# Kernel optimization log

Hardware: AMD Instinct MI355X
Metric: run time of the kernel (lower is better)

Reference implementation:

```python
import jax, jax.numpy as jnp
import numpy as np
from jax import lax

DN = ('NCH', 'OIH', 'NCH')

def conv1d(x, w, b, pad=0):
    y = lax.conv_general_dilated(x, w, window_strides=(1,), padding=[(pad, pad)], dimension_numbers=DN)
    return y + b[None, :, None]

def conv_transpose1d(x, w_torch, b):
    # torch ConvTranspose1d weight: [C_in, C_out, K]; equivalent to full conv with flipped kernel
    k = w_torch.shape[-1]
    w = jnp.flip(jnp.transpose(w_torch, (1, 0, 2)), axis=-1)  # [C_out, C_in, K]
    y = lax.conv_general_dilated(x, w, window_strides=(1,), padding=[(k - 1, k - 1)], dimension_numbers=DN)
    return y + b[None, :, None]

def converter(signal, w1, b1, w2, b2, wt, bt, w3, b3):
    h = jax.nn.relu(conv1d(signal, w1, b1))          # [B,10,n-2]
    h = jax.nn.relu(conv1d(h, w2, b2))               # [B,10,n-2]
    h = jax.nn.relu(conv_transpose1d(h, wt, bt))     # [B,10,n]
    h = jax.nn.sigmoid(conv1d(h, w3, b3))            # [B,2,n]
    return h

def setup_inputs() -> dict:
    key = jax.random.key(0)
    ks = jax.random.split(key, 12)
    B, C, n = 32, 128, 8192
    signal = jax.random.normal(ks[0], (B, C, n), dtype=jnp.float32)
    curr_diag = jax.random.uniform(ks[1], (B, n - 1), dtype=jnp.float32) + 0.5
    s = 0.1
    return {
        'signal': signal,
        'curr_diag': curr_diag,
        'index_diag': 1,
        'w1': jax.random.normal(ks[2], (10, C, 3), dtype=jnp.float32) * s,
        'b1': jax.random.normal(ks[3], (10,), dtype=jnp.float32) * s,
        'w2': jax.random.normal(ks[4], (10, 10, 1), dtype=jnp.float32) * s,
        'b2': jax.random.normal(ks[5], (10,), dtype=jnp.float32) * s,
        'wt': jax.random.normal(ks[6], (10, 10, 3), dtype=jnp.float32) * s,
        'bt': jax.random.normal(ks[7], (10,), dtype=jnp.float32) * s,
        'w3': jax.random.normal(ks[8], (2, 10, 1), dtype=jnp.float32) * s,
        'b3': jax.random.normal(ks[9], (2,), dtype=jnp.float32) * s,
        'const': jnp.float32(0.99),
    }

def reference(signal, curr_diag, index_diag, w1, b1, w2, b2, wt, bt, w3, b3, const):
    n = signal.shape[-1]
    lr = converter(signal, w1, b1, w2, b2, wt, bt, w3, b3)  # [B,2,n]
    left, right = lr[:, 0, :], lr[:, 1, :]
    # diag_len = n - index_diag; next diag has length diag_len - 1
    mass_in = curr_diag[:, 1:] * right[:, 1:n - index_diag]
    mass_in = mass_in + curr_diag[:, :-1] * left[:, index_diag:n - 1]
    mass_out = right[:, 0:n - index_diag - 1] + left[:, index_diag + 1:n]
    next_diag = const * mass_in / mass_out
    next_diag = jnp.log(next_diag)
    next_diag = next_diag - jnp.mean(next_diag)
    return next_diag
```

## Files before the change

### kernel.cpp

```cpp
#include <hip/hip_runtime.h>
#include <math.h>

#define B    32
#define CIN  128
#define NN   8192
#define N1   8190
#define N1P  8192
#define CH   10

__global__ void k0_prep(const float* __restrict__ w1, float* __restrict__ wT)
{
    const int i = blockIdx.x * 256 + threadIdx.x;
    if (i < CIN * 32) {
        const int ci = i >> 5, r = i & 31;
        float v = 0.f;
        if (r < 30) {
            const int o = r / 3, k = r - o * 3;
            v = w1[(o * CIN + ci) * 3 + k];
        }
        wT[i] = v;
    }
}

__global__ __launch_bounds__(256) void k1_conv12(
    const float* __restrict__ sig, const float* __restrict__ wT, const float* __restrict__ b1,
    const float* __restrict__ w2, const float* __restrict__ b2, float* __restrict__ h2out)
{
    const int tid = threadIdx.x;
    const int b   = blockIdx.y;
    const int t   = blockIdx.x * 256 + tid;
    const int tc  = (t < N1 - 1) ? t : (N1 - 1);
    const float* sp = sig + (size_t)b * CIN * NN + tc;

    float y[CH];
#pragma unroll
    for (int o = 0; o < CH; ++o) y[o] = b1[o];

    float ax[8], ay[8], az[8];
    float bx[8], by[8], bz[8];

    auto load = [&](float* x0, float* x1, float* x2, int c) {
#pragma unroll
        for (int j = 0; j < 8; ++j) {
            const float* p = sp + (size_t)(c * 8 + j) * NN;
            x0[j] = p[0]; x1[j] = p[1]; x2[j] = p[2];
        }
    };
    auto comp = [&](const float* x0, const float* x1, const float* x2, int c) {
        const float* wbase = wT + c * 8 * 32;
#pragma unroll
        for (int j = 0; j < 8; ++j) {
            const float* wrow = wbase + j * 32;
#pragma unroll
            for (int o = 0; o < CH; ++o) {
                y[o] = fmaf(wrow[o * 3 + 0], x0[j], y[o]);
                y[o] = fmaf(wrow[o * 3 + 1], x1[j], y[o]);
                y[o] = fmaf(wrow[o * 3 + 2], x2[j], y[o]);
            }
        }
    };

    load(ax, ay, az, 0);
    for (int c = 0; c < 16; c += 2) {
        load(bx, by, bz, c + 1);
        comp(ax, ay, az, c);
        if (c + 2 < 16) load(ax, ay, az, c + 2);
        comp(bx, by, bz, c + 1);
    }

    if (t < N1) {
#pragma unroll
        for (int o = 0; o < CH; ++o) y[o] = fmaxf(y[o], 0.f);
#pragma unroll
        for (int o = 0; o < CH; ++o) {
            float a = b2[o];
#pragma unroll
            for (int i = 0; i < CH; ++i) a = fmaf(w2[o * CH + i], y[i], a);
            h2out[((size_t)b * CH + o) * N1P + t] = fmaxf(a, 0.f);
        }
    }
}

__global__ __launch_bounds__(256) void k2_fused(
    const float* __restrict__ h2, const float* __restrict__ cd,
    const float* __restrict__ wt, const float* __restrict__ bt,
    const float* __restrict__ w3, const float* __restrict__ b3,
    const float* __restrict__ cstp, float* __restrict__ outv, float* __restrict__ bsums)
{
    __shared__ float lsh[260], rsh[260];
    __shared__ float red[256];
    const int tid = threadIdx.x;
    const int b   = blockIdx.y;
    const int t0  = blockIdx.x * 256;
    const float* hb = h2 + (size_t)b * CH * N1P;

    auto computeLR = [&](int sidx) {
        const int s = t0 + sidx;
        float acc[CH];
#pragma unroll
        for (int o = 0; o < CH; ++o) acc[o] = bt[o];
#pragma unroll
        for (int i = 0; i < CH; ++i) {
            const float* hp = hb + (size_t)i * N1P;
            const float v0 = (s < N1)            ? hp[s]     : 0.f;
            const float v1 = (s >= 1 && s <= N1) ? hp[s - 1] : 0.f;
            const float v2 = (s >= 2)            ? hp[s - 2] : 0.f;
            const float* wp = wt + i * CH * 3;
#pragma unroll
            for (int o = 0; o < CH; ++o) {
                acc[o] = fmaf(wp[o * 3 + 0], v0, acc[o]);
                acc[o] = fmaf(wp[o * 3 + 1], v1, acc[o]);
                acc[o] = fmaf(wp[o * 3 + 2], v2, acc[o]);
            }
        }
        float l = b3[0], r = b3[1];
#pragma unroll
        for (int o = 0; o < CH; ++o) {
            const float h3 = fmaxf(acc[o], 0.f);
            l = fmaf(w3[o],      h3, l);
            r = fmaf(w3[CH + o], h3, r);
        }
        lsh[sidx] = 1.f / (1.f + __expf(-l));
        rsh[sidx] = 1.f / (1.f + __expf(-r));
    };

    computeLR(tid);
    if (tid < 3 && t0 + 256 + tid < NN) computeLR(256 + tid);
    __syncthreads();

    const int t = t0 + tid;
    float v = 0.f;
    if (t < N1) {
        const float c0 = cd[(size_t)b * (NN - 1) + t];
        const float c1 = cd[(size_t)b * (NN - 1) + t + 1];
        const float mi = c1 * rsh[tid + 1] + c0 * lsh[tid + 1];
        const float mo = rsh[tid] + lsh[tid + 2];
        v = __logf(cstp[0] * mi / mo);
        outv[(size_t)b * N1 + t] = v;
    }

    red[tid] = v;
    __syncthreads();
#pragma unroll
    for (int s = 128; s > 0; s >>= 1) {
        if (tid < s) red[tid] += red[tid + s];
        __syncthreads();
    }
    if (tid == 0) bsums[blockIdx.y * gridDim.x + blockIdx.x] = red[0];
}

__global__ __launch_bounds__(256) void k3_meansub(
    const float* __restrict__ bsums, float* __restrict__ outv, int n)
{
    __shared__ float red[256];
    const int tid = threadIdx.x;
    float s = 0.f;
#pragma unroll
    for (int i = 0; i < 4; ++i) s += bsums[tid + i * 256];
    red[tid] = s;
    __syncthreads();
#pragma unroll
    for (int st = 128; st > 0; st >>= 1) {
        if (tid < st) red[tid] += red[tid + st];
        __syncthreads();
    }
    const float mean = red[0] / (float)(B * N1);
    __syncthreads();
    const int i = blockIdx.x * 256 + tid;
    if (i < n) outv[i] -= mean;
}

extern "C" void kernel_launch(void* const* d_in, const int* in_sizes, int n_in,
                              void* d_out, int out_size, void* d_ws, size_t ws_size,
                              hipStream_t stream)
{
    const float* sig = (const float*)d_in[0];
    const float* cd  = (const float*)d_in[1];
    const float* w1  = (const float*)d_in[3];
    const float* b1  = (const float*)d_in[4];
    const float* w2  = (const float*)d_in[5];
    const float* b2  = (const float*)d_in[6];
    const float* wt  = (const float*)d_in[7];
    const float* bt  = (const float*)d_in[8];
    const float* w3  = (const float*)d_in[9];
    const float* b3  = (const float*)d_in[10];
    const float* cst = (const float*)d_in[11];

    float* outv = (float*)d_out;

    float* ws   = (float*)d_ws;
    float* wT   = ws;
    float* h2   = wT + CIN * 32;
    float* bsum = h2 + (size_t)B * CH * N1P;

    dim3 blk(256);
    dim3 g1(32, B);

    k0_prep   <<<dim3(16), blk, 0, stream>>>(w1, wT);
    k1_conv12 <<<g1, blk, 0, stream>>>(sig, wT, b1, w2, b2, h2);
    k2_fused  <<<g1, blk, 0, stream>>>(h2, cd, wt, bt, w3, b3, cst, outv, bsum);
    k3_meansub<<<dim3((out_size + 255) / 256), blk, 0, stream>>>(bsum, outv, out_size);
}
```

Measured before the change: 265.1 us.

## Fuse conv1/conv2 with transpose-conv and output stage using halo tiles in LDS

```diff
diff --git a/kernel.cpp b/kernel.cpp
--- a/kernel.cpp
+++ b/kernel.cpp
@@ -1,12 +1,13 @@
 #include <hip/hip_runtime.h>
 #include <math.h>
 
-#define B    32
-#define CIN  128
-#define NN   8192
-#define N1   8190
-#define N1P  8192
-#define CH   10
+#define B     32
+#define CIN   128
+#define NN    8192
+#define N1    8190
+#define CH    10
+#define TOUT  252
+#define NTILE 33
 
 __global__ void k0_prep(const float* __restrict__ w1, float* __restrict__ wT)
 {
@@ -22,95 +23,81 @@
     }
 }
 
-__global__ __launch_bounds__(256) void k1_conv12(
-    const float* __restrict__ sig, const float* __restrict__ wT, const float* __restrict__ b1,
-    const float* __restrict__ w2, const float* __restrict__ b2, float* __restrict__ h2out)
+__global__ __launch_bounds__(256, 4) void k_main(
+    const float* __restrict__ sig, const float* __restrict__ wT,
+    const float* __restrict__ b1, const float* __restrict__ w2, const float* __restrict__ b2,
+    const float* __restrict__ wt, const float* __restrict__ bt,
+    const float* __restrict__ w3, const float* __restrict__ b3,
+    const float* __restrict__ cd, const float* __restrict__ cstp,
+    float* __restrict__ outv, float* __restrict__ bsums)
 {
+    __shared__ float h2s[CH * 256];
+    __shared__ float lsh[256], rsh[256];
+    __shared__ float red[256];
+
     const int tid = threadIdx.x;
     const int b   = blockIdx.y;
-    const int t   = blockIdx.x * 256 + tid;
-    const int tc  = (t < N1 - 1) ? t : (N1 - 1);
-    const float* sp = sig + (size_t)b * CIN * NN + tc;
+    const int t0  = blockIdx.x * TOUT;
+    const int g   = t0 - 2 + tid;
+    const bool gvalid = (g >= 0) && (g < N1);
+    const bool sh = (g > NN - 4);
+    int gl = (g < 0) ? 0 : g;
+    if (gl > NN - 4) gl = NN - 4;
+    const float* sb = sig + (size_t)b * CIN * NN + gl;
 
     float y[CH];
 #pragma unroll
     for (int o = 0; o < CH; ++o) y[o] = b1[o];
 
-    float ax[8], ay[8], az[8];
-    float bx[8], by[8], bz[8];
+    for (int c = 0; c < 8; ++c) {
+        float4 v[16];
+#pragma unroll
+        for (int j = 0; j < 16; ++j)
+            v[j] = *(const float4*)(sb + (size_t)(c * 16 + j) * NN);
 
-    auto load = [&](float* x0, float* x1, float* x2, int c) {
+        const float* wbase = wT + c * 16 * 32;
 #pragma unroll
-        for (int j = 0; j < 8; ++j) {
-            const float* p = sp + (size_t)(c * 8 + j) * NN;
-            x0[j] = p[0]; x1[j] = p[1]; x2[j] = p[2];
-        }
-    };
-    auto comp = [&](const float* x0, const float* x1, const float* x2, int c) {
-        const float* wbase = wT + c * 8 * 32;
-#pragma unroll
-        for (int j = 0; j < 8; ++j) {
+        for (int j = 0; j < 16; ++j) {
+            const float s0 = sh ? v[j].y : v[j].x;
+            const float s1 = sh ? v[j].z : v[j].y;
+            const float s2 = sh ? v[j].w : v[j].z;
             const float* wrow = wbase + j * 32;
 #pragma unroll
             for (int o = 0; o < CH; ++o) {
-                y[o] = fmaf(wrow[o * 3 + 0], x0[j], y[o]);
-                y[o] = fmaf(wrow[o * 3 + 1], x1[j], y[o]);
-                y[o] = fmaf(wrow[o * 3 + 2], x2[j], y[o]);
+                y[o] = fmaf(wrow[o * 3 + 0], s0, y[o]);
+                y[o] = fmaf(wrow[o * 3 + 1], s1, y[o]);
+                y[o] = fmaf(wrow[o * 3 + 2], s2, y[o]);
             }
         }
-    };
-
-    load(ax, ay, az, 0);
-    for (int c = 0; c < 16; c += 2) {
-        load(bx, by, bz, c + 1);
-        comp(ax, ay, az, c);
-        if (c + 2 < 16) load(ax, ay, az, c + 2);
-        comp(bx, by, bz, c + 1);
     }
 
-    if (t < N1) {
 #pragma unroll
-        for (int o = 0; o < CH; ++o) y[o] = fmaxf(y[o], 0.f);
+    for (int o = 0; o < CH; ++o) y[o] = fmaxf(y[o], 0.f);
 #pragma unroll
-        for (int o = 0; o < CH; ++o) {
-            float a = b2[o];
+    for (int o = 0; o < CH; ++o) {
+        float a = b2[o];
 #pragma unroll
-            for (int i = 0; i < CH; ++i) a = fmaf(w2[o * CH + i], y[i], a);
-            h2out[((size_t)b * CH + o) * N1P + t] = fmaxf(a, 0.f);
-        }
+        for (int i = 0; i < CH; ++i) a = fmaf(w2[o * CH + i], y[i], a);
+        h2s[o * 256 + tid] = gvalid ? fmaxf(a, 0.f) : 0.f;
     }
-}
+    __syncthreads();
 
-__global__ __launch_bounds__(256) void k2_fused(
-    const float* __restrict__ h2, const float* __restrict__ cd,
-    const float* __restrict__ wt, const float* __restrict__ bt,
-    const float* __restrict__ w3, const float* __restrict__ b3,
-    const float* __restrict__ cstp, float* __restrict__ outv, float* __restrict__ bsums)
-{
-    __shared__ float lsh[260], rsh[260];
-    __shared__ float red[256];
-    const int tid = threadIdx.x;
-    const int b   = blockIdx.y;
-    const int t0  = blockIdx.x * 256;
-    const float* hb = h2 + (size_t)b * CH * N1P;
-
-    auto computeLR = [&](int sidx) {
-        const int s = t0 + sidx;
+    const int s = t0 + tid;
+    if (tid < 254 && s < NN) {
         float acc[CH];
 #pragma unroll
         for (int o = 0; o < CH; ++o) acc[o] = bt[o];
 #pragma unroll
         for (int i = 0; i < CH; ++i) {
-            const float* hp = hb + (size_t)i * N1P;
-            const float v0 = (s < N1)            ? hp[s]     : 0.f;
-            const float v1 = (s >= 1 && s <= N1) ? hp[s - 1] : 0.f;
-            const float v2 = (s >= 2)            ? hp[s - 2] : 0.f;
+            const float a0 = h2s[i * 256 + tid];
+            const float a1 = h2s[i * 256 + tid + 1];
+            const float a2 = h2s[i * 256 + tid + 2];
             const float* wp = wt + i * CH * 3;
 #pragma unroll
             for (int o = 0; o < CH; ++o) {
-                acc[o] = fmaf(wp[o * 3 + 0], v0, acc[o]);
-                acc[o] = fmaf(wp[o * 3 + 1], v1, acc[o]);
-                acc[o] = fmaf(wp[o * 3 + 2], v2, acc[o]);
+                acc[o] = fmaf(wp[o * 3 + 0], a2, acc[o]);
+                acc[o] = fmaf(wp[o * 3 + 1], a1, acc[o]);
+                acc[o] = fmaf(wp[o * 3 + 2], a0, acc[o]);
             }
         }
         float l = b3[0], r = b3[1];
@@ -120,33 +107,30 @@
             l = fmaf(w3[o],      h3, l);
             r = fmaf(w3[CH + o], h3, r);
         }
-        lsh[sidx] = 1.f / (1.f + __expf(-l));
-        rsh[sidx] = 1.f / (1.f + __expf(-r));
-    };
-
-    computeLR(tid);
-    if (tid < 3 && t0 + 256 + tid < NN) computeLR(256 + tid);
+        lsh[tid] = 1.f / (1.f + __expf(-l));
+        rsh[tid] = 1.f / (1.f + __expf(-r));
+    }
     __syncthreads();
 
+    float vlog = 0.f;
     const int t = t0 + tid;
-    float v = 0.f;
-    if (t < N1) {
+    if (tid < TOUT && t < N1) {
         const float c0 = cd[(size_t)b * (NN - 1) + t];
         const float c1 = cd[(size_t)b * (NN - 1) + t + 1];
         const float mi = c1 * rsh[tid + 1] + c0 * lsh[tid + 1];
         const float mo = rsh[tid] + lsh[tid + 2];
-        v = __logf(cstp[0] * mi / mo);
-        outv[(size_t)b * N1 + t] = v;
+        vlog = __logf(cstp[0] * mi / mo);
+        outv[(size_t)b * N1 + t] = vlog;
     }
 
-    red[tid] = v;
+    red[tid] = vlog;
     __syncthreads();
 #pragma unroll
-    for (int s = 128; s > 0; s >>= 1) {
-        if (tid < s) red[tid] += red[tid + s];
+    for (int st = 128; st > 0; st >>= 1) {
+        if (tid < st) red[tid] += red[tid + st];
         __syncthreads();
     }
-    if (tid == 0) bsums[blockIdx.y * gridDim.x + blockIdx.x] = red[0];
+    if (tid == 0) bsums[blockIdx.y * NTILE + blockIdx.x] = red[0];
 }
 
 __global__ __launch_bounds__(256) void k3_meansub(
@@ -155,8 +139,7 @@
     __shared__ float red[256];
     const int tid = threadIdx.x;
     float s = 0.f;
-#pragma unroll
-    for (int i = 0; i < 4; ++i) s += bsums[tid + i * 256];
+    for (int i = tid; i < NTILE * B; i += 256) s += bsums[i];
     red[tid] = s;
     __syncthreads();
 #pragma unroll
@@ -190,14 +173,12 @@
 
     float* ws   = (float*)d_ws;
     float* wT   = ws;
-    float* h2   = wT + CIN * 32;
-    float* bsum = h2 + (size_t)B * CH * N1P;
+    float* bsum = wT + CIN * 32;
 
     dim3 blk(256);
-    dim3 g1(32, B);
 
     k0_prep   <<<dim3(16), blk, 0, stream>>>(w1, wT);
-    k1_conv12 <<<g1, blk, 0, stream>>>(sig, wT, b1, w2, b2, h2);
-    k2_fused  <<<g1, blk, 0, stream>>>(h2, cd, wt, bt, w3, b3, cst, outv, bsum);
+    k_main    <<<dim3(NTILE, B), blk, 0, stream>>>(sig, wT, b1, w2, b2,
+                                                   wt, bt, w3, b3, cd, cst, outv, bsum);
     k3_meansub<<<dim3((out_size + 255) / 256), blk, 0, stream>>>(bsum, outv, out_size);
 }
```

New measurement: 243.8 us. -8.0%, faster.
